# Kernel tuning notes

Measured on AMD Instinct MI355X. Metric: run time of the kernel, lower is better.

## Reference

```python
import jax, jax.numpy as jnp
import numpy as np

HEADS = 8
DIM_HEAD = 64
SCALE = DIM_HEAD ** -0.5


def setup_inputs() -> dict:
    key = jax.random.key(0)
    k1, k2, k3 = jax.random.split(key, 3)
    b, seq, dim = 4, 8192, 512
    inner = HEADS * DIM_HEAD  # 512
    x = jax.random.normal(k1, (b, seq, dim), dtype=jnp.float32)
    w_qkv = jax.random.normal(k2, (dim, 3 * inner), dtype=jnp.float32) * (dim ** -0.5)
    w_out = jax.random.normal(k3, (inner, dim), dtype=jnp.float32) * (inner ** -0.5)
    b_out = jnp.zeros((dim,), dtype=jnp.float32)
    return {"x": x, "w_qkv": w_qkv, "w_out": w_out, "b_out": b_out, "f": 32}


def reference(x, w_qkv, w_out, b_out, f):
    b, seq, dim = x.shape
    h, dh = HEADS, DIM_HEAD
    n_sp = seq // f  # spatial tokens per frame

    qkv = jnp.einsum('bnd,de->bne', x, w_qkv)  # [b, seq, 3*inner]
    q, k, v = jnp.split(qkv, 3, axis=-1)

    def to_axial(t):
        # 'b n (h d) -> (b h) n d' then 'b (f n) d -> (b f) n d'
        t = t.reshape(b, seq, h, dh).transpose(0, 2, 1, 3)  # [b, h, seq, dh]
        return t.reshape(b * h * f, n_sp, dh)               # [(b h f), n_sp, dh]

    q = to_axial(q) * SCALE
    k = to_axial(k)
    v = to_axial(v)

    sim = jnp.einsum('bid,bjd->bij', q, k)      # [(b h f), n_sp, n_sp]
    attn = jax.nn.softmax(sim, axis=-1)
    out = jnp.einsum('bij,bjd->bid', attn, v)   # [(b h f), n_sp, dh]

    # reverse: '(b f) n d -> b (f n) d' then '(b h) n d -> b n (h d)'
    out = out.reshape(b, h, seq, dh).transpose(0, 2, 1, 3).reshape(b, seq, h * dh)
    return jnp.einsum('bne,ed->bnd', out, w_out) + b_out
```

## Files before the change

### kernel.cpp

```cpp
#include <hip/hip_runtime.h>
#include <hip/hip_bf16.h>
#include <cstdint>

using bf16x8 = __attribute__((ext_vector_type(8))) short;
using f32x4  = __attribute__((ext_vector_type(4))) float;
using f32x16 = __attribute__((ext_vector_type(16))) float;

typedef const __attribute__((address_space(1))) void* gas_ptr;
typedef __attribute__((address_space(3))) void* lds_ptr;

#define M_ROWS 32768
#define PLANE ((size_t)M_ROWS * 64)

__device__ __forceinline__ short f2bf(float f) {
  unsigned u = __builtin_bit_cast(unsigned, f);
  u += 0x7fffu + ((u >> 16) & 1u);
  return (short)(u >> 16);
}

__device__ __forceinline__ unsigned pack2(float a, float b) {
  unsigned ua = __builtin_bit_cast(unsigned, a);
  ua += 0x7fffu + ((ua >> 16) & 1u);
  unsigned ub = __builtin_bit_cast(unsigned, b);
  ub += 0x7fffu + ((ub >> 16) & 1u);
  return (ua >> 16) | (ub & 0xffff0000u);
}

__global__ __launch_bounds__(256) void convert_bf16(const float* __restrict__ src,
                                                    short* __restrict__ dst, int n8) {
  int i = blockIdx.x * 256 + threadIdx.x;
  if (i >= n8) return;
  const float4* s = (const float4*)(src + (size_t)i * 8);
  float4 a = s[0], b = s[1];
  uint4 o;
  o.x = pack2(a.x, a.y); o.y = pack2(a.z, a.w);
  o.z = pack2(b.x, b.y); o.w = pack2(b.z, b.w);
  *(uint4*)(dst + (size_t)i * 8) = o;
}

__global__ __launch_bounds__(256) void transpose_to_bf16(const float* __restrict__ src,
                                                         short* __restrict__ dst,
                                                         int R, int C) {
  int idx = blockIdx.x * 256 + threadIdx.x;
  if (idx >= R * C) return;
  int c = idx / R;
  int r = idx - c * R;
  dst[(size_t)c * R + r] = f2bf(src[(size_t)r * C + c]);
}

template <int MODE>
__device__ __forceinline__ void gemm8p_body(const short* __restrict__ A,
                                            const short* __restrict__ Bt,
                                            void* __restrict__ Cp,
                                            const float* __restrict__ bias,
                                            int Mt, int Nt, int N) {
  constexpr int K  = 512;
  constexpr int NT = K / 64;
  __shared__ short lds[65536];

  const int tid  = threadIdx.x;
  const int lane = tid & 63;
  const int w    = tid >> 6;
  const int c16  = lane & 15;
  const int g    = lane >> 4;
  const int wm   = w >> 2;
  const int wn   = w & 3;

  const int nwg = gridDim.x;
  const int bid = blockIdx.x;
  const int swz = (bid & 7) * (nwg >> 3) + (bid >> 3);
  const int mtile = swz / Nt;
  const int ntile = swz % Nt;
  const int m0 = mtile * 256;
  const int n0 = ntile * 256;

  const int stg_r = w * 16 + (lane >> 2);
  const int stg_c = ((lane & 3) ^ ((lane >> 3) & 3)) * 8;
  const short* gA = (MODE == 1)
      ? A + (size_t)(m0 + stg_r) * 64 + stg_c
      : A + (size_t)(m0 + stg_r) * K + stg_c;
  const short* gB = Bt + (size_t)(n0 + stg_r) * K + stg_c;
  short* const ldsA = lds;
  short* const ldsB = lds + 32768;
  const int stg_d = w * 512;

  const int f_lane = c16 * 32 + ((g ^ ((c16 >> 1) & 3)) * 8);

  f32x4 acc[2][4][4] = {};
  bf16x8 bf[4], af[4];

#define STG_(isA, p, kh, tile) do {                                               \
    short* _d = ((isA) ? ldsA : ldsB) + ((p) * 2 + (kh)) * 8192 + stg_d;          \
    if ((isA) && MODE == 1) {                                                     \
      const short* _s = gA + (size_t)(tile) * PLANE + (kh) * 32;                  \
      __builtin_amdgcn_global_load_lds((gas_ptr)_s, (lds_ptr)_d, 16, 0, 0);       \
      __builtin_amdgcn_global_load_lds((gas_ptr)(_s + 128 * 64), (lds_ptr)(_d + 4096), 16, 0, 0); \
    } else {                                                                      \
      const short* _s = ((isA) ? gA : gB) + (tile) * 64 + (kh) * 32;              \
      __builtin_amdgcn_global_load_lds((gas_ptr)_s, (lds_ptr)_d, 16, 0, 0);       \
      __builtin_amdgcn_global_load_lds((gas_ptr)(_s + 128 * K), (lds_ptr)(_d + 4096), 16, 0, 0); \
    }                                                                             \
  } while (0)

  STG_(1, 0, 0, 0); STG_(0, 0, 0, 0);
  STG_(1, 0, 1, 0); STG_(0, 0, 1, 0);
  STG_(1, 1, 0, 1); STG_(0, 1, 0, 1);
  asm volatile("s_waitcnt vmcnt(4)" ::: "memory");
  __builtin_amdgcn_s_barrier();
  asm volatile("" ::: "memory");

#define PHASE_(p, mq, kh, LOADB, sisA, sp, skh, stile, DOVM) do {                 \
    if (LOADB) {                                                                  \
      _Pragma("unroll")                                                           \
      for (int nf = 0; nf < 4; nf++)                                              \
        bf[nf] = *(const bf16x8*)&ldsB[((p) * 2 + (kh)) * 8192 +                  \
                                       (wn * 64 + nf * 16) * 32 + f_lane];        \
    }                                                                             \
    _Pragma("unroll")                                                             \
    for (int mf = 0; mf < 4; mf++)                                                \
      af[mf] = *(const bf16x8*)&ldsA[((p) * 2 + (kh)) * 8192 +                    \
                                     (wm * 128 + (mq) * 64 + mf * 16) * 32 + f_lane]; \
    STG_(sisA, sp, skh, stile);                                                   \
    asm volatile("" ::: "memory");                                                \
    __builtin_amdgcn_s_barrier();                                                 \
    __builtin_amdgcn_s_setprio(1);                                                \
    _Pragma("unroll")                                                             \
    for (int mf = 0; mf < 4; mf++)                                                \
      _Pragma("unroll")                                                           \
      for (int nf = 0; nf < 4; nf++)                                              \
        acc[mq][mf][nf] = __builtin_amdgcn_mfma_f32_16x16x32_bf16(af[mf], bf[nf], \
                                                      acc[mq][mf][nf], 0, 0, 0);  \
    __builtin_amdgcn_s_setprio(0);                                                \
    if (DOVM) asm volatile("s_waitcnt vmcnt(4)" ::: "memory");                    \
    asm volatile("" ::: "memory");                                                \
    __builtin_amdgcn_s_barrier();                                                 \
    asm volatile("" ::: "memory");                                                \
  } while (0)

  for (int j = 0; j < NT / 2; j++) {
    const int u  = 2 * j;
    const int t1 = u + 1;
    const int t2 = (u + 2 < NT) ? u + 2 : NT - 1;
    const int t3 = (u + 3 < NT) ? u + 3 : NT - 1;
    PHASE_(0, 0, 0, 1,  1, 1, 1, t1, 0);
    PHASE_(0, 1, 0, 0,  0, 1, 1, t1, 0);
    PHASE_(0, 0, 1, 1,  1, 0, 0, t2, 0);
    PHASE_(0, 1, 1, 0,  0, 0, 0, t2, 1);
    PHASE_(1, 0, 0, 1,  1, 0, 1, t2, 0);
    PHASE_(1, 1, 0, 0,  0, 0, 1, t2, 0);
    PHASE_(1, 0, 1, 1,  1, 1, 0, t3, 0);
    PHASE_(1, 1, 1, 0,  0, 1, 0, t3, 1);
  }
#undef PHASE_
#undef STG_

  asm volatile("s_waitcnt vmcnt(0)" ::: "memory");
  __builtin_amdgcn_s_barrier();

  if (MODE == 0) {
    #pragma unroll
    for (int mq = 0; mq < 2; mq++)
      #pragma unroll
      for (int mf = 0; mf < 4; mf++)
        #pragma unroll
        for (int nf = 0; nf < 4; nf++) {
          const int row = wm * 128 + mq * 64 + mf * 16 + g * 4;
          const int col = wn * 64 + nf * 16 + c16;
          #pragma unroll
          for (int r = 0; r < 4; r++)
            lds[(row + r) * 256 + col] = f2bf(acc[mq][mf][nf][r]);
        }
    __syncthreads();
    #pragma unroll
    for (int cg = 0; cg < 4; cg++) {
      const int colbase = n0 + cg * 64;
      const int plane = (colbase >> 9) * 8 + ((colbase >> 6) & 7);
      short* op = (short*)Cp + (size_t)plane * PLANE + (size_t)m0 * 64;
      #pragma unroll
      for (int ps = 0; ps < 4; ps++) {
        const int row = ps * 128 + (tid >> 2);
        const int sc  = (tid & 3) * 16;
        (void)sc;
        const int row8 = ps * 64 + (tid >> 3);
        const int sc8  = (tid & 7) * 8;
        *(uint4*)(op + (size_t)row8 * 64 + sc8) =
            *(const uint4*)&lds[row8 * 256 + cg * 64 + sc8];
        (void)row;
      }
    }
  } else {
    #pragma unroll
    for (int mq = 0; mq < 2; mq++) {
      #pragma unroll
      for (int mf = 0; mf < 4; mf++) {
        #pragma unroll
        for (int nf = 0; nf < 4; nf++) {
          const int row = m0 + wm * 128 + mq * 64 + mf * 16 + g * 4;
          const int col = n0 + wn * 64 + nf * 16 + c16;
          float* C = (float*)Cp;
          const float bb = bias ? bias[col] : 0.f;
          #pragma unroll
          for (int r = 0; r < 4; r++)
            C[(size_t)(row + r) * N + col] = acc[mq][mf][nf][r] + bb;
        }
      }
    }
  }
}

__global__ __launch_bounds__(512, 2) void gemm8p_qkv(const short* __restrict__ A,
                                                     const short* __restrict__ Bt,
                                                     void* __restrict__ Cp,
                                                     int Mt, int Nt, int N) {
  gemm8p_body<0>(A, Bt, Cp, nullptr, Mt, Nt, N);
}
__global__ __launch_bounds__(512, 2) void gemm8p_out(const short* __restrict__ A,
                                                     const short* __restrict__ Bt,
                                                     void* __restrict__ Cp,
                                                     const float* __restrict__ bias,
                                                     int Mt, int Nt, int N) {
  gemm8p_body<1>(A, Bt, Cp, bias, Mt, Nt, N);
}

__global__ __launch_bounds__(512, 2) void attn_kernel(const short* __restrict__ qkv,
                                                      short* __restrict__ attn_out) {
  __shared__ short Kl[256 * 64];
  __shared__ short Vr[256 * 64];

  const int tid    = threadIdx.x;
  const int lane   = tid & 63;
  const int w      = tid >> 6;
  const int lane31 = lane & 31;
  const int hi     = lane >> 5;

  const int bid = blockIdx.x;
  const int fr  = bid & 31;
  const int h   = (bid >> 5) & 7;
  const int bb  = bid >> 8;
  const size_t rowbase = (size_t)bb * 8192 + (size_t)fr * 256;
  const short* qp = qkv + (size_t)(0 + h) * PLANE + rowbase * 64;
  const short* kp = qkv + (size_t)(8 + h) * PLANE + rowbase * 64;
  const short* vp = qkv + (size_t)(16 + h) * PLANE + rowbase * 64;

  #pragma unroll
  for (int j = 0; j < 4; j++) {
    const int g  = j * 512 + tid;
    const int r  = g >> 3;
    const int sl = g & 7;
    const int off = r * 128 + ((sl ^ (r & 7)) << 4);
    uint4 kc = *(const uint4*)(kp + (size_t)g * 8);
    *(uint4*)((char*)Kl + off) = kc;
    uint4 vc = *(const uint4*)(vp + (size_t)g * 8);
    *(uint4*)((char*)Vr + off) = vc;
  }
  __syncthreads();

  {
    const int p   = tid & 127;
    const int grp = tid >> 7;
    const int r0 = 2 * p, r1 = 2 * p + 1;
    bf16x8 ta[2], tb[2];
    #pragma unroll
    for (int i = 0; i < 2; i++) {
      const int cb = grp * 32 + i * 16;
      ta[i] = *(const bf16x8*)((const char*)Vr + r0 * 128 + (cb ^ ((r0 & 7) << 4)));
      tb[i] = *(const bf16x8*)((const char*)Vr + r1 * 128 + (cb ^ ((r1 & 7) << 4)));
    }
    __syncthreads();
    #pragma unroll
    for (int i = 0; i < 2; i++) {
      #pragma unroll
      for (int k = 0; k < 8; k++) {
        const int d = grp * 16 + i * 8 + k;
        unsigned pk = ((unsigned)(unsigned short)ta[i][k]) |
                      (((unsigned)(unsigned short)tb[i][k]) << 16);
        *(unsigned*)((char*)Vr + d * 512 + ((4 * p) ^ ((d & 7) << 4))) = pk;
      }
    }
  }
  __syncthreads();

  const int swl = (lane31 & 7) << 4;
  const int q0  = w * 32;
  unsigned pko[16];

  {
    const short* qrow = qp + (size_t)(q0 + lane31) * 64;
    bf16x8 qf[4];
    #pragma unroll
    for (int ds = 0; ds < 4; ds++)
      qf[ds] = *(const bf16x8*)(qrow + ds * 16 + 8 * hi);

    f32x16 o0 = {}, o1 = {};
    float m = 0.f, l = 0.f;

    #pragma unroll
    for (int j = 0; j < 4; j++) {
      f32x16 sA = {}, sB = {};
      __builtin_amdgcn_s_setprio(1);
      #pragma unroll
      for (int ds = 0; ds < 4; ds++) {
        bf16x8 kfA = *(const bf16x8*)((const char*)Kl + (j * 64 + lane31) * 128 +
                                      ((ds * 32 + 16 * hi) ^ swl));
        sA = __builtin_amdgcn_mfma_f32_32x32x16_bf16(kfA, qf[ds], sA, 0, 0, 0);
        bf16x8 kfB = *(const bf16x8*)((const char*)Kl + (j * 64 + 32 + lane31) * 128 +
                                      ((ds * 32 + 16 * hi) ^ swl));
        sB = __builtin_amdgcn_mfma_f32_32x32x16_bf16(kfB, qf[ds], sB, 0, 0, 0);
      }
      __builtin_amdgcn_s_setprio(0);

      float tm[16];
      #pragma unroll
      for (int r = 0; r < 16; r++) tm[r] = fmaxf(sA[r], sB[r]);
      #pragma unroll
      for (int st = 8; st > 0; st >>= 1)
        #pragma unroll
        for (int r = 0; r < 8; r++)
          if (r < st) tm[r] = fmaxf(tm[r], tm[r + st]);
      float bm = fmaxf(tm[0], __shfl_xor(tm[0], 32));

      if (j == 0) {
        m = bm;
      } else if (!__all((bm - m) <= 64.f)) {
        const float mnew = fmaxf(m, bm);
        const float corr = __expf((m - mnew) * 0.125f);
        #pragma unroll
        for (int r = 0; r < 16; r++) { o0[r] *= corr; o1[r] *= corr; }
        l *= corr;
        m = mnew;
      }

      float ts[16];
      #pragma unroll
      for (int r = 0; r < 16; r++) {
        sA[r] = __expf((sA[r] - m) * 0.125f);
        sB[r] = __expf((sB[r] - m) * 0.125f);
        ts[r] = sA[r] + sB[r];
      }
      #pragma unroll
      for (int st = 8; st > 0; st >>= 1)
        #pragma unroll
        for (int r = 0; r < 8; r++)
          if (r < st) ts[r] += ts[r + st];
      l += ts[0] + __shfl_xor(ts[0], 32);

#define PVBLK(SV, rb, mm) do {                                                     \
        unsigned u0 = pack2(SV[(rb) + 0], SV[(rb) + 1]);                           \
        unsigned u1 = pack2(SV[(rb) + 2], SV[(rb) + 3]);                           \
        unsigned u2 = pack2(SV[(rb) + 4], SV[(rb) + 5]);                           \
        unsigned u3 = pack2(SV[(rb) + 6], SV[(rb) + 7]);                           \
        int s0 = hi ? (int)u0 : (int)u2;                                           \
        int s1 = hi ? (int)u1 : (int)u3;                                           \
        int r0 = __shfl_xor(s0, 32);                                               \
        int r1 = __shfl_xor(s1, 32);                                               \
        int4 paw;                                                                  \
        paw.x = hi ? r0 : (int)u0;                                                 \
        paw.y = hi ? r1 : (int)u1;                                                 \
        paw.z = hi ? (int)u2 : r0;                                                 \
        paw.w = hi ? (int)u3 : r1;                                                 \
        bf16x8 pa = __builtin_bit_cast(bf16x8, paw);                               \
        bf16x8 v0f = *(const bf16x8*)((const char*)Vr + (size_t)lane31 * 512 +     \
                                      (((mm) * 32 + 16 * hi) ^ swl));              \
        bf16x8 v1f = *(const bf16x8*)((const char*)Vr + (size_t)(32 + lane31) * 512 + \
                                      (((mm) * 32 + 16 * hi) ^ swl));              \
        o0 = __builtin_amdgcn_mfma_f32_32x32x16_bf16(v0f, pa, o0, 0, 0, 0);        \
        o1 = __builtin_amdgcn_mfma_f32_32x32x16_bf16(v1f, pa, o1, 0, 0, 0);        \
      } while (0)

      PVBLK(sA, 0, j * 4 + 0);
      PVBLK(sA, 8, j * 4 + 1);
      PVBLK(sB, 0, j * 4 + 2);
      PVBLK(sB, 8, j * 4 + 3);
#undef PVBLK
    }

    const float inv = 1.0f / l;
    #pragma unroll
    for (int r = 0; r < 16; r++) { o0[r] *= inv; o1[r] *= inv; }
    #pragma unroll
    for (int g2 = 0; g2 < 4; g2++) {
      pko[2 * g2 + 0] = pack2(o0[4 * g2 + 0], o0[4 * g2 + 1]);
      pko[2 * g2 + 1] = pack2(o0[4 * g2 + 2], o0[4 * g2 + 3]);
      pko[8 + 2 * g2 + 0] = pack2(o1[4 * g2 + 0], o1[4 * g2 + 1]);
      pko[8 + 2 * g2 + 1] = pack2(o1[4 * g2 + 2], o1[4 * g2 + 3]);
    }
  }

  __syncthreads();
  {
    const int row = q0 + lane31;
    const int rx  = (row & 7) << 4;
    #pragma unroll
    for (int g2 = 0; g2 < 4; g2++) {
      uint2 a, b;
      a.x = pko[2 * g2 + 0]; a.y = pko[2 * g2 + 1];
      b.x = pko[8 + 2 * g2 + 0]; b.y = pko[8 + 2 * g2 + 1];
      *(uint2*)((char*)Kl + row * 128 + ((16 * g2 + 8 * hi) ^ rx))      = a;
      *(uint2*)((char*)Kl + row * 128 + ((64 + 16 * g2 + 8 * hi) ^ rx)) = b;
    }
  }
  __syncthreads();
  short* op = attn_out + (size_t)h * PLANE + rowbase * 64;
  #pragma unroll
  for (int j = 0; j < 4; j++) {
    const int row = j * 64 + (tid >> 3);
    const int sl  = tid & 7;
    uint4 v = *(const uint4*)((const char*)Kl + row * 128 + ((sl << 4) ^ ((row & 7) << 4)));
    *(uint4*)(op + (size_t)row * 64 + sl * 8) = v;
  }
}

extern "C" void kernel_launch(void* const* d_in, const int* in_sizes, int n_in,
                              void* d_out, int out_size, void* d_ws, size_t ws_size,
                              hipStream_t stream) {
  const float* x     = (const float*)d_in[0];
  const float* w_qkv = (const float*)d_in[1];
  const float* w_out = (const float*)d_in[2];
  const float* b_out = (const float*)d_in[3];
  float* out = (float*)d_out;

  const int M = M_ROWS, DIM = 512, NQKV = 1536;

  short* wqkvT = (short*)d_ws;
  short* woutT = wqkvT + (size_t)NQKV * DIM;
  short* qkvb  = woutT + (size_t)DIM * DIM;
  short* attnb = qkvb + (size_t)M * NQKV;
  short* xbf   = attnb;

  transpose_to_bf16<<<(DIM * NQKV + 255) / 256, 256, 0, stream>>>(w_qkv, wqkvT, DIM, NQKV);
  transpose_to_bf16<<<(DIM * DIM + 255) / 256, 256, 0, stream>>>(w_out, woutT, DIM, DIM);
  convert_bf16<<<(M * DIM / 8 + 255) / 256, 256, 0, stream>>>(x, xbf, M * DIM / 8);

  gemm8p_qkv<<<(M / 256) * (NQKV / 256), 512, 0, stream>>>(xbf, wqkvT, qkvb,
                                                           M / 256, NQKV / 256, NQKV);

  attn_kernel<<<1024, 512, 0, stream>>>(qkvb, attnb);

  gemm8p_out<<<(M / 256) * (DIM / 256), 512, 0, stream>>>(attnb, woutT, out, b_out,
                                                          M / 256, DIM / 256, DIM);
}
```

Measured before the change: 165.9 us.

## Swizzle GEMM epilogue LDS, stage fp32 output through LDS, hoist Q loads

The QKV GEMM epilogue now XOR-swizzles its LDS staging columns to reduce bank conflicts. The output GEMM epilogue now stages fp32 accumulators plus bias through LDS in two halves, so each row is written with coalesced 16-byte stores instead of scattered scalar stores. The attention kernel issues its Q fragment loads before the K/V staging so they overlap, and the bf16 conversion kernel becomes a grid-stride loop with a fixed grid. The changes add extra LDS traffic and barriers in the out-GEMM epilogue and keep Q registers live longer in attention.

```diff
diff --git a/kernel.cpp b/kernel.cpp
--- a/kernel.cpp
+++ b/kernel.cpp
@@ -28,14 +28,14 @@
 
 __global__ __launch_bounds__(256) void convert_bf16(const float* __restrict__ src,
                                                     short* __restrict__ dst, int n8) {
-  int i = blockIdx.x * 256 + threadIdx.x;
-  if (i >= n8) return;
-  const float4* s = (const float4*)(src + (size_t)i * 8);
-  float4 a = s[0], b = s[1];
-  uint4 o;
-  o.x = pack2(a.x, a.y); o.y = pack2(a.z, a.w);
-  o.z = pack2(b.x, b.y); o.w = pack2(b.z, b.w);
-  *(uint4*)(dst + (size_t)i * 8) = o;
+  for (int i = blockIdx.x * 256 + threadIdx.x; i < n8; i += gridDim.x * 256) {
+    const float4* s = (const float4*)(src + (size_t)i * 8);
+    float4 a = s[0], b = s[1];
+    uint4 o;
+    o.x = pack2(a.x, a.y); o.y = pack2(a.z, a.w);
+    o.z = pack2(b.x, b.y); o.w = pack2(b.z, b.w);
+    *(uint4*)(dst + (size_t)i * 8) = o;
+  }
 }
 
 __global__ __launch_bounds__(256) void transpose_to_bf16(const float* __restrict__ src,
@@ -167,8 +167,10 @@
           const int row = wm * 128 + mq * 64 + mf * 16 + g * 4;
           const int col = wn * 64 + nf * 16 + c16;
           #pragma unroll
-          for (int r = 0; r < 4; r++)
-            lds[(row + r) * 256 + col] = f2bf(acc[mq][mf][nf][r]);
+          for (int r = 0; r < 4; r++) {
+            const int rr = row + r;
+            lds[rr * 256 + (col ^ (((rr >> 2) & 3) << 4))] = f2bf(acc[mq][mf][nf][r]);
+          }
         }
     __syncthreads();
     #pragma unroll
@@ -178,31 +180,40 @@
       short* op = (short*)Cp + (size_t)plane * PLANE + (size_t)m0 * 64;
       #pragma unroll
       for (int ps = 0; ps < 4; ps++) {
-        const int row = ps * 128 + (tid >> 2);
-        const int sc  = (tid & 3) * 16;
-        (void)sc;
         const int row8 = ps * 64 + (tid >> 3);
         const int sc8  = (tid & 7) * 8;
+        const int colL = cg * 64 + sc8;
         *(uint4*)(op + (size_t)row8 * 64 + sc8) =
-            *(const uint4*)&lds[row8 * 256 + cg * 64 + sc8];
-        (void)row;
+            *(const uint4*)&lds[row8 * 256 + (colL ^ (((row8 >> 2) & 3) << 4))];
       }
     }
   } else {
-    #pragma unroll
-    for (int mq = 0; mq < 2; mq++) {
-      #pragma unroll
-      for (int mf = 0; mf < 4; mf++) {
+    float* ldsf = (float*)lds;
+    float* C = (float*)Cp;
+    #pragma unroll
+    for (int p = 0; p < 2; p++) {
+      if (p) __syncthreads();
+      #pragma unroll
+      for (int mf = 0; mf < 4; mf++)
         #pragma unroll
         for (int nf = 0; nf < 4; nf++) {
-          const int row = m0 + wm * 128 + mq * 64 + mf * 16 + g * 4;
-          const int col = n0 + wn * 64 + nf * 16 + c16;
-          float* C = (float*)Cp;
-          const float bb = bias ? bias[col] : 0.f;
+          const int lrow = wm * 64 + mf * 16 + g * 4;
+          const int col  = wn * 64 + nf * 16 + c16;
+          const float bb = bias ? bias[n0 + col] : 0.f;
           #pragma unroll
-          for (int r = 0; r < 4; r++)
-            C[(size_t)(row + r) * N + col] = acc[mq][mf][nf][r] + bb;
+          for (int r = 0; r < 4; r++) {
+            const int rr = lrow + r;
+            ldsf[rr * 256 + (col ^ (((rr >> 2) & 3) << 4))] = acc[p][mf][nf][r] + bb;
+          }
         }
+      __syncthreads();
+      #pragma unroll
+      for (int jj = 0; jj < 16; jj++) {
+        const int lr   = jj * 8 + (tid >> 6);
+        const int coff = (tid & 63) * 4;
+        uint4 v = *(const uint4*)&ldsf[lr * 256 + (coff ^ (((lr >> 2) & 3) << 4))];
+        const int grow = m0 + (lr >> 6) * 128 + p * 64 + (lr & 63);
+        *(uint4*)&C[(size_t)grow * N + n0 + coff] = v;
       }
     }
   }
@@ -241,6 +252,14 @@
   const short* qp = qkv + (size_t)(0 + h) * PLANE + rowbase * 64;
   const short* kp = qkv + (size_t)(8 + h) * PLANE + rowbase * 64;
   const short* vp = qkv + (size_t)(16 + h) * PLANE + rowbase * 64;
+
+  const int q0 = w * 32;
+
+  const short* qrow = qp + (size_t)(q0 + lane31) * 64;
+  bf16x8 qf[4];
+  #pragma unroll
+  for (int ds = 0; ds < 4; ds++)
+    qf[ds] = *(const bf16x8*)(qrow + ds * 16 + 8 * hi);
 
   #pragma unroll
   for (int j = 0; j < 4; j++) {
@@ -281,16 +300,9 @@
   __syncthreads();
 
   const int swl = (lane31 & 7) << 4;
-  const int q0  = w * 32;
   unsigned pko[16];
 
   {
-    const short* qrow = qp + (size_t)(q0 + lane31) * 64;
-    bf16x8 qf[4];
-    #pragma unroll
-    for (int ds = 0; ds < 4; ds++)
-      qf[ds] = *(const bf16x8*)(qrow + ds * 16 + 8 * hi);
-
     f32x16 o0 = {}, o1 = {};
     float m = 0.f, l = 0.f;
 
@@ -429,7 +441,7 @@
 
   transpose_to_bf16<<<(DIM * NQKV + 255) / 256, 256, 0, stream>>>(w_qkv, wqkvT, DIM, NQKV);
   transpose_to_bf16<<<(DIM * DIM + 255) / 256, 256, 0, stream>>>(w_out, woutT, DIM, DIM);
-  convert_bf16<<<(M * DIM / 8 + 255) / 256, 256, 0, stream>>>(x, xbf, M * DIM / 8);
+  convert_bf16<<<2048, 256, 0, stream>>>(x, xbf, M * DIM / 8);
 
   gemm8p_qkv<<<(M / 256) * (NQKV / 256), 512, 0, stream>>>(xbf, wqkvT, qkvb,
                                                            M / 256, NQKV / 256, NQKV);
```

New measurement: 168.4 us. About the same (+1.5%).
